# Optimization experiments

Measured on AMD Instinct MI355X. Metric: run time of the kernel, lower is better.

## Reference

```python
import jax, jax.numpy as jnp
import numpy as np

B, S, D, H = 4, 2048, 1024, 16
HD = D // H


def setup_inputs() -> dict:
    key = jax.random.key(0)
    ks = jax.random.split(key, 12)
    inp = {
        'query': jax.random.normal(ks[0], (B, S, D), jnp.float32),
        'key': jax.random.normal(ks[1], (B, S, D), jnp.float32),
        'value': jax.random.normal(ks[2], (B, S, D), jnp.float32),
        'mask': jnp.ones((B, 1, 1, S), jnp.bool_),
        # nn.Linear weights are [out, in]; y = x @ W.T + b
        'Wq': jax.random.normal(ks[3], (D, D), jnp.float32) * 0.02,
        'bq': jnp.zeros((D,), jnp.float32),
        'Wk': jax.random.normal(ks[4], (D, D), jnp.float32) * 0.02,
        'bk': jnp.zeros((D,), jnp.float32),
        'Wv': jax.random.normal(ks[5], (D, D), jnp.float32) * 0.02,
        'bv': jnp.zeros((D,), jnp.float32),
        'Wo': jax.random.normal(ks[6], (D, D), jnp.float32) * 0.02,
        'bo': jnp.zeros((D,), jnp.float32),
    }
    return inp


def reference(query, key, value, mask, Wq, bq, Wk, bk, Wv, bv, Wo, bo):
    scale = 1.0 / np.sqrt(HD).astype(np.float32)

    def proj(x, W, b):
        # [B,S,D] -> [B,H,S,HD]
        y = x @ W.T + b
        return y.reshape(B, S, H, HD).transpose(0, 2, 1, 3)

    q = proj(query, Wq, bq)
    k = proj(key, Wk, bk)
    v = proj(value, Wv, bv)
    # scores: [B,H,S,S]
    scores = jnp.einsum('bhqd,bhkd->bhqk', q, k) * scale
    scores = jnp.where(mask, scores, -jnp.inf)
    attn = jax.nn.softmax(scores, axis=-1)  # dropout p=0 in eval
    ctx = jnp.einsum('bhqk,bhkd->bhqd', attn, v)  # [B,H,S,HD]
    ctx = ctx.transpose(0, 2, 1, 3).reshape(B, S, D)
    return ctx @ Wo.T + bo
```

## Files before the change

### kernel.cpp

```cpp
#include <hip/hip_runtime.h>
#include <hip/hip_bf16.h>

#define SCLOG (0.125f * 1.4426950408889634f)

typedef __attribute__((ext_vector_type(8))) short short8;
typedef __attribute__((ext_vector_type(4))) short s16x4;
typedef __attribute__((ext_vector_type(4))) float f32x4;

__device__ __forceinline__ short f2bf(float f) {
    __hip_bfloat16 h = __float2bfloat16(f);
    short s;
    __builtin_memcpy(&s, &h, 2);
    return s;
}

__device__ __forceinline__ void gl_lds16(const void* g, void* l) {
    __builtin_amdgcn_global_load_lds(
        (const __attribute__((address_space(1))) unsigned int*)g,
        (__attribute__((address_space(3))) unsigned int*)l,
        16, 0, 0);
}

__global__ __launch_bounds__(256) void cvt3(
    const float* __restrict__ a, const float* __restrict__ b,
    const float* __restrict__ c, short* __restrict__ oa,
    short* __restrict__ ob, short* __restrict__ oc, int n8)
{
    int i = blockIdx.x * 256 + threadIdx.x;
    if (i >= n8) return;
    const float* in = blockIdx.y == 0 ? a : (blockIdx.y == 1 ? b : c);
    short* out = blockIdx.y == 0 ? oa : (blockIdx.y == 1 ? ob : oc);
    float4 v0 = ((const float4*)in)[2 * i];
    float4 v1 = ((const float4*)in)[2 * i + 1];
    short8 s = { f2bf(v0.x), f2bf(v0.y), f2bf(v0.z), f2bf(v0.w),
                 f2bf(v1.x), f2bf(v1.y), f2bf(v1.z), f2bf(v1.w) };
    *(short8*)(out + 8 * (size_t)i) = s;
}

__global__ __launch_bounds__(256) void cvt4(
    const float* __restrict__ a, const float* __restrict__ b,
    const float* __restrict__ c, const float* __restrict__ d,
    short* __restrict__ oa, short* __restrict__ ob,
    short* __restrict__ oc, short* __restrict__ od, int n8)
{
    int i = blockIdx.x * 256 + threadIdx.x;
    if (i >= n8) return;
    const float* in = blockIdx.y == 0 ? a : (blockIdx.y == 1 ? b :
                      (blockIdx.y == 2 ? c : d));
    short* out = blockIdx.y == 0 ? oa : (blockIdx.y == 1 ? ob :
                 (blockIdx.y == 2 ? oc : od));
    float4 v0 = ((const float4*)in)[2 * i];
    float4 v1 = ((const float4*)in)[2 * i + 1];
    short8 s = { f2bf(v0.x), f2bf(v0.y), f2bf(v0.z), f2bf(v0.w),
                 f2bf(v1.x), f2bf(v1.y), f2bf(v1.z), f2bf(v1.w) };
    *(short8*)(out + 8 * (size_t)i) = s;
}

template<int NZ, bool OUT_BF16, bool VTOUT>
__global__ __launch_bounds__(256) void gemm_bt_bf16(
    const short* __restrict__ A0, const short* __restrict__ A1,
    const short* __restrict__ A2,
    const short* __restrict__ W0, const short* __restrict__ W1,
    const short* __restrict__ W2,
    const float* __restrict__ b0, const float* __restrict__ b1,
    const float* __restrict__ b2,
    short* __restrict__ C0, short* __restrict__ C1, short* __restrict__ C2,
    void* __restrict__ Cf, int M, int N, int K)
{
    __shared__ short As[128 * 64];
    __shared__ short Bs[128 * 64];
    const int tid = threadIdx.x;
    const int wave = tid >> 6, lane = tid & 63;
    const int quad = lane >> 4, l16 = lane & 15;
    const int wm = (wave >> 1) * 64, wn = (wave & 1) * 64;
    const int bm0 = blockIdx.y * 128, bn0 = blockIdx.x * 128;
    const int rowA = lane >> 3;
    const int chunkS = (((lane & 7) ^ rowA) * 8);
    const int rsw = (l16 & 7);

    const short* A; const short* W; const float* bias; short* Cb;
    if constexpr (NZ == 3) {
        A    = blockIdx.z == 0 ? A0 : (blockIdx.z == 1 ? A1 : A2);
        W    = blockIdx.z == 0 ? W0 : (blockIdx.z == 1 ? W1 : W2);
        bias = blockIdx.z == 0 ? b0 : (blockIdx.z == 1 ? b1 : b2);
        Cb   = blockIdx.z == 0 ? C0 : (blockIdx.z == 1 ? C1 : C2);
    } else {
        A = A0; W = W0; bias = b0; Cb = C0;
    }

    const short* Ab = A + (size_t)bm0 * K;
    const short* Wb = W + (size_t)bn0 * K;

    f32x4 acc[4][4] = {};

    for (int kt = 0; kt < K; kt += 64) {
        #pragma unroll
        for (int i = 0; i < 4; ++i) {
            int r0 = wave * 32 + i * 8;
            gl_lds16(Ab + (size_t)(r0 + rowA) * K + kt + chunkS, As + r0 * 64);
            gl_lds16(Wb + (size_t)(r0 + rowA) * K + kt + chunkS, Bs + r0 * 64);
        }
        __syncthreads();

        #pragma unroll
        for (int h = 0; h < 2; ++h) {
            const int slot = ((h * 4 + quad) ^ rsw) * 8;
            short8 af[4], bf[4];
            #pragma unroll
            for (int mi = 0; mi < 4; ++mi)
                af[mi] = *(const short8*)(As + (wm + mi * 16 + l16) * 64 + slot);
            #pragma unroll
            for (int ni = 0; ni < 4; ++ni)
                bf[ni] = *(const short8*)(Bs + (wn + ni * 16 + l16) * 64 + slot);
            #pragma unroll
            for (int mi = 0; mi < 4; ++mi)
                #pragma unroll
                for (int ni = 0; ni < 4; ++ni)
                    acc[mi][ni] = __builtin_amdgcn_mfma_f32_16x16x32_bf16(
                        af[mi], bf[ni], acc[mi][ni], 0, 0, 0);
        }
        __syncthreads();
    }

    bool vt_mode = false;
    if constexpr (VTOUT) vt_mode = (blockIdx.z == 2);

    if (vt_mode) {
        const int SS = 2048;
        const int bidx = bm0 >> 11;
        const int s0b  = (bm0 & 2047) + wm;
        #pragma unroll
        for (int ni = 0; ni < 4; ++ni) {
            int n = bn0 + wn + ni * 16 + l16;
            float bb = bias[n];
            int hh = n >> 6, dd = n & 63;
            short* vrow = Cb + ((size_t)((bidx * 16 + hh) * 64 + dd)) * SS;
            #pragma unroll
            for (int mi = 0; mi < 4; ++mi) {
                int s0 = s0b + mi * 16 + quad * 4;
                s16x4 pk = { f2bf(acc[mi][ni][0] + bb), f2bf(acc[mi][ni][1] + bb),
                             f2bf(acc[mi][ni][2] + bb), f2bf(acc[mi][ni][3] + bb) };
                *(s16x4*)(vrow + s0) = pk;
            }
        }
    } else {
        #pragma unroll
        for (int ni = 0; ni < 4; ++ni) {
            int n = bn0 + wn + ni * 16 + l16;
            float bb = bias[n];
            #pragma unroll
            for (int mi = 0; mi < 4; ++mi)
                #pragma unroll
                for (int r = 0; r < 4; ++r) {
                    int m = bm0 + wm + mi * 16 + quad * 4 + r;
                    float v = acc[mi][ni][r] + bb;
                    if constexpr (OUT_BF16)
                        Cb[(size_t)m * N + n] = f2bf(v);
                    else
                        ((float*)Cf)[(size_t)m * N + n] = v;
                }
        }
    }
}

__global__ __launch_bounds__(256) void flash_attn(
    const short* __restrict__ Q, const short* __restrict__ Kb,
    const short* __restrict__ VT, const int* __restrict__ mask,
    short* __restrict__ Ctx)
{
    const int S = 2048, D = 1024;
    __shared__ short Ks[2][64 * 64];
    __shared__ short Vs[2][64 * 64];
    __shared__ short Ps[4][32 * 72];

    const int tid = threadIdx.x;
    const int wave = tid >> 6, lane = tid & 63;
    const int quad = lane >> 4, l16 = lane & 15;
    const int q0 = blockIdx.x * 128 + wave * 32;
    const int head = blockIdx.y, b = blockIdx.z;
    const size_t qbase  = ((size_t)(b * S)) * D + head * 64;
    const size_t vtbase = ((size_t)((b * 16 + head) * 64)) * S;
    const int rowA = lane >> 3;
    const int chunkS = (((lane & 7) ^ rowA) * 8);
    const int rsw = (l16 & 7);

    short8 qf[2][2];
    #pragma unroll
    for (int qi = 0; qi < 2; ++qi)
        #pragma unroll
        for (int h = 0; h < 2; ++h)
            qf[qi][h] = *(const short8*)(Q + qbase + (size_t)(q0 + qi * 16 + l16) * D + h * 32 + quad * 8);

    f32x4 o[2][4] = {};
    f32x4 osum[2] = {};
    const short8 ones = { (short)0x3F80, (short)0x3F80, (short)0x3F80, (short)0x3F80,
                          (short)0x3F80, (short)0x3F80, (short)0x3F80, (short)0x3F80 };

    const int* mrow = mask + (size_t)b * S;
    short* Pw = Ps[wave];
    const int slot0 = (quad ^ rsw) * 8;
    const int slot1 = ((4 + quad) ^ rsw) * 8;

    auto STAGE = [&](int kts, int bufi) {
        const int r0 = wave * 16;
        gl_lds16(Kb + qbase + (size_t)(kts + r0 + rowA) * D + chunkS,      &Ks[bufi][r0 * 64]);
        gl_lds16(Kb + qbase + (size_t)(kts + r0 + 8 + rowA) * D + chunkS,  &Ks[bufi][(r0 + 8) * 64]);
        gl_lds16(VT + vtbase + (size_t)(r0 + rowA) * S + kts + chunkS,     &Vs[bufi][r0 * 64]);
        gl_lds16(VT + vtbase + (size_t)(r0 + 8 + rowA) * S + kts + chunkS, &Vs[bufi][(r0 + 8) * 64]);
    };

    STAGE(0, 0);
    __syncthreads();

    for (int kt = 0; kt < S; kt += 64) {
        const int cur = (kt >> 6) & 1;
        if (kt + 64 < S) STAGE(kt + 64, cur ^ 1);

        const short* Kc = &Ks[cur][0];
        const short* Vc = &Vs[cur][0];

        float p[2][4][4];
        #pragma unroll
        for (int t = 0; t < 4; ++t) {
            short8 kf0 = *(const short8*)(Kc + (t * 16 + l16) * 64 + slot0);
            short8 kf1 = *(const short8*)(Kc + (t * 16 + l16) * 64 + slot1);
            float mb = mrow[kt + t * 16 + l16] != 0 ? 0.f : -1e30f;
            #pragma unroll
            for (int qi = 0; qi < 2; ++qi) {
                f32x4 a = {};
                a = __builtin_amdgcn_mfma_f32_16x16x32_bf16(qf[qi][0], kf0, a, 0, 0, 0);
                a = __builtin_amdgcn_mfma_f32_16x16x32_bf16(qf[qi][1], kf1, a, 0, 0, 0);
                #pragma unroll
                for (int r = 0; r < 4; ++r)
                    p[qi][t][r] = __builtin_amdgcn_exp2f(__builtin_fmaf(a[r], SCLOG, mb));
            }
        }

        #pragma unroll
        for (int qi = 0; qi < 2; ++qi)
            #pragma unroll
            for (int t = 0; t < 4; ++t)
                #pragma unroll
                for (int r = 0; r < 4; ++r)
                    Pw[(qi * 16 + quad * 4 + r) * 72 + t * 16 + l16] = f2bf(p[qi][t][r]);

        __builtin_amdgcn_s_setprio(1);
        #pragma unroll
        for (int h = 0; h < 2; ++h) {
            const int vslot = ((h * 4 + quad) ^ rsw) * 8;
            short8 pa0 = *(const short8*)(Pw + l16 * 72 + h * 32 + quad * 8);
            short8 pa1 = *(const short8*)(Pw + (16 + l16) * 72 + h * 32 + quad * 8);
            osum[0] = __builtin_amdgcn_mfma_f32_16x16x32_bf16(pa0, ones, osum[0], 0, 0, 0);
            osum[1] = __builtin_amdgcn_mfma_f32_16x16x32_bf16(pa1, ones, osum[1], 0, 0, 0);
            #pragma unroll
            for (int nt = 0; nt < 4; ++nt) {
                short8 bv = *(const short8*)(Vc + (nt * 16 + l16) * 64 + vslot);
                o[0][nt] = __builtin_amdgcn_mfma_f32_16x16x32_bf16(pa0, bv, o[0][nt], 0, 0, 0);
                o[1][nt] = __builtin_amdgcn_mfma_f32_16x16x32_bf16(pa1, bv, o[1][nt], 0, 0, 0);
            }
        }
        __builtin_amdgcn_s_setprio(0);
        __syncthreads();
    }

    float inv[2][4];
    #pragma unroll
    for (int qi = 0; qi < 2; ++qi)
        #pragma unroll
        for (int r = 0; r < 4; ++r)
            inv[qi][r] = 1.0f / osum[qi][r];

    #pragma unroll
    for (int qi = 0; qi < 2; ++qi)
        #pragma unroll
        for (int nt = 0; nt < 4; ++nt)
            #pragma unroll
            for (int r = 0; r < 4; ++r) {
                float v = o[qi][nt][r] * inv[qi][r];
                Ctx[qbase + (size_t)(q0 + qi * 16 + quad * 4 + r) * D + nt * 16 + l16] = f2bf(v);
            }
}

extern "C" void kernel_launch(void* const* d_in, const int* in_sizes, int n_in,
                              void* d_out, int out_size, void* d_ws, size_t ws_size,
                              hipStream_t stream) {
    const int B = 4, S = 2048, D = 1024, H = 16;
    const int M = B * S;
    const size_t MD = (size_t)M * D;

    const float* q_in = (const float*)d_in[0];
    const float* k_in = (const float*)d_in[1];
    const float* v_in = (const float*)d_in[2];
    const int* mask = (const int*)d_in[3];
    const float* Wq = (const float*)d_in[4];
    const float* bq = (const float*)d_in[5];
    const float* Wk = (const float*)d_in[6];
    const float* bk = (const float*)d_in[7];
    const float* Wv = (const float*)d_in[8];
    const float* bv = (const float*)d_in[9];
    const float* Wo = (const float*)d_in[10];
    const float* bo = (const float*)d_in[11];

    short* S1 = (short*)d_ws;
    short* S2 = S1 + MD;
    short* S3 = S2 + MD;
    short* S4 = S3 + MD;
    short* wqb = S4 + MD;
    short* wkb = wqb + (size_t)D * D;
    short* wvb = wkb + (size_t)D * D;
    short* wob = wvb + (size_t)D * D;
    short* S5 = wob + (size_t)D * D;
    short* S6 = S5 + MD;

    short *qbf = S1, *kbf = S2, *vbf = S3;
    short *Qb = S4, *Kb2 = S5, *VTb = S6, *Ctx = S2;

    dim3 blk(256);
    int n8_in = (int)(MD / 8);
    int n8_w  = D * D / 8;
    cvt3<<<dim3((n8_in + 255) / 256, 3), blk, 0, stream>>>(
        q_in, k_in, v_in, qbf, kbf, vbf, n8_in);
    cvt4<<<dim3((n8_w + 255) / 256, 4), blk, 0, stream>>>(
        Wq, Wk, Wv, Wo, wqb, wkb, wvb, wob, n8_w);

    dim3 g1(D / 128, M / 128, 3);
    gemm_bt_bf16<3, true, true><<<g1, blk, 0, stream>>>(
        qbf, kbf, vbf, wqb, wkb, wvb, bq, bk, bv,
        Qb, Kb2, VTb, nullptr, M, D, D);

    dim3 g2(S / 128, H, B);
    flash_attn<<<g2, blk, 0, stream>>>(Qb, Kb2, VTb, mask, Ctx);

    dim3 g3(D / 128, M / 128, 1);
    gemm_bt_bf16<1, false, false><<<g3, blk, 0, stream>>>(
        Ctx, nullptr, nullptr, wob, nullptr, nullptr, bo, nullptr, nullptr,
        nullptr, nullptr, nullptr, (float*)d_out, M, D, D);
}
```

Before: 390.2 us.

## Pass softmax probabilities via cross-lane shuffles instead of LDS round-trip

The flash attention kernel now computes S^T by swapping the MFMA operand order, so each lane holds four consecutive keys for one query. It packs the exp2 results into bf16 pairs and rebuilds the P operand for the PV MFMA with ds_bpermute shuffles instead of writing P to shared memory and reading it back. The mask is read as an int4 per lane. This removes the per-wave LDS staging buffer and its scattered 2-byte stores. In exchange it issues 16 shuffles per half-tile plus select instructions, and it uses more registers.

```diff
diff --git a/kernel.cpp b/kernel.cpp
--- a/kernel.cpp
+++ b/kernel.cpp
@@ -12,6 +12,12 @@
     short s;
     __builtin_memcpy(&s, &h, 2);
     return s;
+}
+
+__device__ __forceinline__ unsigned pack2(float a, float b) {
+    unsigned sa = (unsigned)(unsigned short)f2bf(a);
+    unsigned sb = (unsigned)(unsigned short)f2bf(b);
+    return sa | (sb << 16);
 }
 
 __device__ __forceinline__ void gl_lds16(const void* g, void* l) {
@@ -171,7 +177,6 @@
     const int S = 2048, D = 1024;
     __shared__ short Ks[2][64 * 64];
     __shared__ short Vs[2][64 * 64];
-    __shared__ short Ps[4][32 * 72];
 
     const int tid = threadIdx.x;
     const int wave = tid >> 6, lane = tid & 63;
@@ -197,9 +202,12 @@
                           (short)0x3F80, (short)0x3F80, (short)0x3F80, (short)0x3F80 };
 
     const int* mrow = mask + (size_t)b * S;
-    short* Pw = Ps[wave];
     const int slot0 = (quad ^ rsw) * 8;
     const int slot1 = ((4 + quad) ^ rsw) * 8;
+
+    const int srcA = l16 + ((quad & 1) << 5);
+    const int srcB = srcA + 16;
+    const bool selhi = (quad & 2) != 0;
 
     auto STAGE = [&](int kts, int bufi) {
         const int r0 = wave * 16;
@@ -219,44 +227,59 @@
         const short* Kc = &Ks[cur][0];
         const short* Vc = &Vs[cur][0];
 
-        float p[2][4][4];
+        unsigned dw[2][4][2];
         #pragma unroll
         for (int t = 0; t < 4; ++t) {
             short8 kf0 = *(const short8*)(Kc + (t * 16 + l16) * 64 + slot0);
             short8 kf1 = *(const short8*)(Kc + (t * 16 + l16) * 64 + slot1);
-            float mb = mrow[kt + t * 16 + l16] != 0 ? 0.f : -1e30f;
+            int4 m4 = *(const int4*)(mrow + kt + t * 16 + quad * 4);
+            float mb0 = m4.x != 0 ? 0.f : -1e30f;
+            float mb1 = m4.y != 0 ? 0.f : -1e30f;
+            float mb2 = m4.z != 0 ? 0.f : -1e30f;
+            float mb3 = m4.w != 0 ? 0.f : -1e30f;
             #pragma unroll
             for (int qi = 0; qi < 2; ++qi) {
                 f32x4 a = {};
-                a = __builtin_amdgcn_mfma_f32_16x16x32_bf16(qf[qi][0], kf0, a, 0, 0, 0);
-                a = __builtin_amdgcn_mfma_f32_16x16x32_bf16(qf[qi][1], kf1, a, 0, 0, 0);
-                #pragma unroll
-                for (int r = 0; r < 4; ++r)
-                    p[qi][t][r] = __builtin_amdgcn_exp2f(__builtin_fmaf(a[r], SCLOG, mb));
-            }
-        }
-
-        #pragma unroll
-        for (int qi = 0; qi < 2; ++qi)
-            #pragma unroll
-            for (int t = 0; t < 4; ++t)
-                #pragma unroll
-                for (int r = 0; r < 4; ++r)
-                    Pw[(qi * 16 + quad * 4 + r) * 72 + t * 16 + l16] = f2bf(p[qi][t][r]);
+                a = __builtin_amdgcn_mfma_f32_16x16x32_bf16(kf0, qf[qi][0], a, 0, 0, 0);
+                a = __builtin_amdgcn_mfma_f32_16x16x32_bf16(kf1, qf[qi][1], a, 0, 0, 0);
+                float p0 = __builtin_amdgcn_exp2f(__builtin_fmaf(a[0], SCLOG, mb0));
+                float p1 = __builtin_amdgcn_exp2f(__builtin_fmaf(a[1], SCLOG, mb1));
+                float p2 = __builtin_amdgcn_exp2f(__builtin_fmaf(a[2], SCLOG, mb2));
+                float p3 = __builtin_amdgcn_exp2f(__builtin_fmaf(a[3], SCLOG, mb3));
+                dw[qi][t][0] = pack2(p0, p1);
+                dw[qi][t][1] = pack2(p2, p3);
+            }
+        }
 
         __builtin_amdgcn_s_setprio(1);
         #pragma unroll
         for (int h = 0; h < 2; ++h) {
             const int vslot = ((h * 4 + quad) ^ rsw) * 8;
-            short8 pa0 = *(const short8*)(Pw + l16 * 72 + h * 32 + quad * 8);
-            short8 pa1 = *(const short8*)(Pw + (16 + l16) * 72 + h * 32 + quad * 8);
-            osum[0] = __builtin_amdgcn_mfma_f32_16x16x32_bf16(pa0, ones, osum[0], 0, 0, 0);
-            osum[1] = __builtin_amdgcn_mfma_f32_16x16x32_bf16(pa1, ones, osum[1], 0, 0, 0);
+            short8 pa[2];
+            #pragma unroll
+            for (int qi = 0; qi < 2; ++qi) {
+                unsigned aLo0 = __shfl((int)dw[qi][2 * h][0],     srcA, 64);
+                unsigned aLo1 = __shfl((int)dw[qi][2 * h][1],     srcA, 64);
+                unsigned aHi0 = __shfl((int)dw[qi][2 * h + 1][0], srcA, 64);
+                unsigned aHi1 = __shfl((int)dw[qi][2 * h + 1][1], srcA, 64);
+                unsigned bLo0 = __shfl((int)dw[qi][2 * h][0],     srcB, 64);
+                unsigned bLo1 = __shfl((int)dw[qi][2 * h][1],     srcB, 64);
+                unsigned bHi0 = __shfl((int)dw[qi][2 * h + 1][0], srcB, 64);
+                unsigned bHi1 = __shfl((int)dw[qi][2 * h + 1][1], srcB, 64);
+                uint4 w;
+                w.x = selhi ? aHi0 : aLo0;
+                w.y = selhi ? aHi1 : aLo1;
+                w.z = selhi ? bHi0 : bLo0;
+                w.w = selhi ? bHi1 : bLo1;
+                __builtin_memcpy(&pa[qi], &w, 16);
+            }
+            osum[0] = __builtin_amdgcn_mfma_f32_16x16x32_bf16(pa[0], ones, osum[0], 0, 0, 0);
+            osum[1] = __builtin_amdgcn_mfma_f32_16x16x32_bf16(pa[1], ones, osum[1], 0, 0, 0);
             #pragma unroll
             for (int nt = 0; nt < 4; ++nt) {
                 short8 bv = *(const short8*)(Vc + (nt * 16 + l16) * 64 + vslot);
-                o[0][nt] = __builtin_amdgcn_mfma_f32_16x16x32_bf16(pa0, bv, o[0][nt], 0, 0, 0);
-                o[1][nt] = __builtin_amdgcn_mfma_f32_16x16x32_bf16(pa1, bv, o[1][nt], 0, 0, 0);
+                o[0][nt] = __builtin_amdgcn_mfma_f32_16x16x32_bf16(pa[0], bv, o[0][nt], 0, 0, 0);
+                o[1][nt] = __builtin_amdgcn_mfma_f32_16x16x32_bf16(pa[1], bv, o[1][nt], 0, 0, 0);
             }
         }
         __builtin_amdgcn_s_setprio(0);
```

Result: slower. 402.8 us (+3.2%).

## Load K/V fragments directly from global memory, dropping LDS staging and barriers

Applied to the files above, without the earlier changes.

The attention kernel no longer stages K and V tiles into double-buffered shared memory. Each wave now reads its MFMA operand fragments straight from global memory, which removes the per-tile __syncthreads and frees LDS. Launch bounds now request 4 blocks per CU for higher occupancy. In exchange, every wave re-reads the same K/V data that the block used to share, which puts more load on L1/L2 and adds global-load latency with no prefetch overlap.

```diff
diff --git a/kernel.cpp b/kernel.cpp
--- a/kernel.cpp
+++ b/kernel.cpp
@@ -163,14 +163,12 @@
     }
 }
 
-__global__ __launch_bounds__(256) void flash_attn(
+__global__ __launch_bounds__(256, 4) void flash_attn(
     const short* __restrict__ Q, const short* __restrict__ Kb,
     const short* __restrict__ VT, const int* __restrict__ mask,
     short* __restrict__ Ctx)
 {
     const int S = 2048, D = 1024;
-    __shared__ short Ks[2][64 * 64];
-    __shared__ short Vs[2][64 * 64];
     __shared__ short Ps[4][32 * 72];
 
     const int tid = threadIdx.x;
@@ -180,9 +178,6 @@
     const int head = blockIdx.y, b = blockIdx.z;
     const size_t qbase  = ((size_t)(b * S)) * D + head * 64;
     const size_t vtbase = ((size_t)((b * 16 + head) * 64)) * S;
-    const int rowA = lane >> 3;
-    const int chunkS = (((lane & 7) ^ rowA) * 8);
-    const int rsw = (l16 & 7);
 
     short8 qf[2][2];
     #pragma unroll
@@ -198,32 +193,17 @@
 
     const int* mrow = mask + (size_t)b * S;
     short* Pw = Ps[wave];
-    const int slot0 = (quad ^ rsw) * 8;
-    const int slot1 = ((4 + quad) ^ rsw) * 8;
-
-    auto STAGE = [&](int kts, int bufi) {
-        const int r0 = wave * 16;
-        gl_lds16(Kb + qbase + (size_t)(kts + r0 + rowA) * D + chunkS,      &Ks[bufi][r0 * 64]);
-        gl_lds16(Kb + qbase + (size_t)(kts + r0 + 8 + rowA) * D + chunkS,  &Ks[bufi][(r0 + 8) * 64]);
-        gl_lds16(VT + vtbase + (size_t)(r0 + rowA) * S + kts + chunkS,     &Vs[bufi][r0 * 64]);
-        gl_lds16(VT + vtbase + (size_t)(r0 + 8 + rowA) * S + kts + chunkS, &Vs[bufi][(r0 + 8) * 64]);
-    };
-
-    STAGE(0, 0);
-    __syncthreads();
+
+    const short* Kfb = Kb + qbase + (size_t)l16 * D + quad * 8;
+    const short* Vfb = VT + vtbase + (size_t)l16 * S + quad * 8;
 
     for (int kt = 0; kt < S; kt += 64) {
-        const int cur = (kt >> 6) & 1;
-        if (kt + 64 < S) STAGE(kt + 64, cur ^ 1);
-
-        const short* Kc = &Ks[cur][0];
-        const short* Vc = &Vs[cur][0];
-
         float p[2][4][4];
         #pragma unroll
         for (int t = 0; t < 4; ++t) {
-            short8 kf0 = *(const short8*)(Kc + (t * 16 + l16) * 64 + slot0);
-            short8 kf1 = *(const short8*)(Kc + (t * 16 + l16) * 64 + slot1);
+            const short* kr = Kfb + (size_t)(kt + t * 16) * D;
+            short8 kf0 = *(const short8*)(kr);
+            short8 kf1 = *(const short8*)(kr + 32);
             float mb = mrow[kt + t * 16 + l16] != 0 ? 0.f : -1e30f;
             #pragma unroll
             for (int qi = 0; qi < 2; ++qi) {
@@ -247,20 +227,18 @@
         __builtin_amdgcn_s_setprio(1);
         #pragma unroll
         for (int h = 0; h < 2; ++h) {
-            const int vslot = ((h * 4 + quad) ^ rsw) * 8;
             short8 pa0 = *(const short8*)(Pw + l16 * 72 + h * 32 + quad * 8);
             short8 pa1 = *(const short8*)(Pw + (16 + l16) * 72 + h * 32 + quad * 8);
             osum[0] = __builtin_amdgcn_mfma_f32_16x16x32_bf16(pa0, ones, osum[0], 0, 0, 0);
             osum[1] = __builtin_amdgcn_mfma_f32_16x16x32_bf16(pa1, ones, osum[1], 0, 0, 0);
             #pragma unroll
             for (int nt = 0; nt < 4; ++nt) {
-                short8 bv = *(const short8*)(Vc + (nt * 16 + l16) * 64 + vslot);
+                short8 bv = *(const short8*)(Vfb + (size_t)(nt * 16) * S + kt + h * 32);
                 o[0][nt] = __builtin_amdgcn_mfma_f32_16x16x32_bf16(pa0, bv, o[0][nt], 0, 0, 0);
                 o[1][nt] = __builtin_amdgcn_mfma_f32_16x16x32_bf16(pa1, bv, o[1][nt], 0, 0, 0);
             }
         }
         __builtin_amdgcn_s_setprio(0);
-        __syncthreads();
     }
 
     float inv[2][4];
```

Measured after the change: 503.5 us. +29.0%, slower.
